# Optimization experiments

Measured on AMD Instinct MI355X. Metric: run time of the kernel, lower is better.

## Reference

```python
import jax, jax.numpy as jnp
import numpy as np

H = 6      # n_attention_heads
BLK = 64


def adder1x1(x2d, w):
    """AdderNet 1x1 'convolution': Y[co, n] = -sum_ci |x2d[ci, n] - w[co, ci]|.
    Processed in output-channel blocks to bound the abs-diff intermediate.
    x2d: [Ci, N], w: [Co, Ci] -> [Co, N]
    """
    co, ci = w.shape
    wb = w.reshape(co // BLK, BLK, ci)
    def f(wblk):  # wblk: [BLK, Ci] -> [BLK, N]
        return -jnp.sum(jnp.abs(x2d[None, :, :] - wblk[:, :, None]), axis=1)
    return jax.lax.map(f, wb).reshape(co, -1)


def layernorm_all(y, w, b, eps=1e-5):
    # nn.LayerNorm([E, B, S]) applied to [1, E, B, S]: normalize over ALL of E,B,S
    mu = jnp.mean(y)
    var = jnp.mean((y - mu) ** 2)
    return (y - mu) * jax.lax.rsqrt(var + eps) * w + b


def layernorm_last(y, w, b, eps=1e-5):
    mu = jnp.mean(y, axis=-1, keepdims=True)
    var = jnp.mean((y - mu) ** 2, axis=-1, keepdims=True)
    return (y - mu) * jax.lax.rsqrt(var + eps) * w + b


def setup_inputs() -> dict:
    key = jax.random.key(0)
    ks = jax.random.split(key, 14)
    B, S, E = 8, 197, 384
    inp = {
        "x": jax.random.normal(ks[0], (B, S, E), jnp.float32),
        "wq": jax.random.normal(ks[1], (E, E), jnp.float32) * 0.05,
        "wk": jax.random.normal(ks[2], (E, E), jnp.float32) * 0.05,
        "wv": jax.random.normal(ks[3], (E, E), jnp.float32) * 0.05,
        "qln_w": 1.0 + 0.02 * jax.random.normal(ks[4], (E, B, S), jnp.float32),
        "qln_b": 0.02 * jax.random.normal(ks[5], (E, B, S), jnp.float32),
        "kln_w": 1.0 + 0.02 * jax.random.normal(ks[6], (E, B, S), jnp.float32),
        "kln_b": 0.02 * jax.random.normal(ks[7], (E, B, S), jnp.float32),
        "vln_w": 1.0 + 0.02 * jax.random.normal(ks[8], (E, B, S), jnp.float32),
        "vln_b": 0.02 * jax.random.normal(ks[9], (E, B, S), jnp.float32),
        "oln_w": 1.0 + 0.02 * jax.random.normal(ks[10], (E,), jnp.float32),
        "oln_b": 0.02 * jax.random.normal(ks[11], (E,), jnp.float32),
        "fc_w": jax.random.normal(ks[12], (E, E), jnp.float32) * 0.05,
        "fc_b": 0.02 * jax.random.normal(ks[13], (E,), jnp.float32),
    }
    return inp


def reference(x, wq, wk, wv, qln_w, qln_b, kln_w, kln_b, vln_w, vln_b,
              oln_w, oln_b, fc_w, fc_b):
    B, S, E = x.shape
    D = E // H
    scale = (2.0 * D * (1.0 - 2.0 / np.pi)) ** (-0.5)

    # torch: x.reshape(1, E, B, S) on contiguous [B,S,E] is a flat-buffer reshape
    x2d = x.reshape(E, B * S)  # [Ci, N]

    def proj(w, lw, lb):
        y = adder1x1(x2d, w).reshape(E, B, S)          # adder2d 1x1, bias=False
        y = layernorm_all(y, lw, lb)                    # LN over [E,B,S]
        y = y.reshape(B, S, H, D)                       # flat reshape (as torch)
        y = jnp.swapaxes(y, 1, 2)                       # [B,H,S,D]
        return y.reshape(B * H, S, D)

    q = proj(wq, qln_w, qln_b)
    k = proj(wk, kln_w, kln_b)
    v = proj(wv, vln_w, vln_b)

    att = jnp.einsum('bsd,btd->bst', q, k) * scale      # [B*H, S, S]
    att = jax.nn.softmax(att, axis=-1) + jnp.eye(S, dtype=x.dtype)
    o = jnp.einsum('bst,btd->bsd', att, v)              # [B*H, S, D]

    o = jnp.swapaxes(o.reshape(B, H, S, D), 1, 2).reshape(B, S, E)
    o = layernorm_last(o, oln_w, oln_b)
    return o @ fc_w.T + fc_b
```

## Files before the change

### kernel.cpp

```cpp
#include <hip/hip_runtime.h>
#include <math.h>

#ifndef M_PI
#define M_PI 3.14159265358979323846
#endif

#define B_ 8
#define S_ 197
#define E_ 384
#define H_ 6
#define D_ 64
#define N_ (B_*S_)
#define EN ((size_t)E_*N_)
#define NBLK_RED 591

__global__ __launch_bounds__(256) void k_adder(
    const float* __restrict__ x,
    const float* __restrict__ wq, const float* __restrict__ wk,
    const float* __restrict__ wv,
    float* __restrict__ P)
{
  const int z = blockIdx.z;
  const int p = z >> 2, c = z & 3;
  const float* __restrict__ w = (p == 0) ? wq : (p == 1) ? wk : wv;
  const int co0 = blockIdx.x * 64;
  const int n0  = blockIdx.y * 64;
  const int cib = c * 96;

  __shared__ float Xs[2][16][68];
  __shared__ float Ws[2][16][68];

  const int tid = threadIdx.x;
  const int tx = tid & 15;
  const int ty = tid >> 4;

  const int xr = tid >> 4, xc = (tid & 15) * 4;
  const int wr = tid >> 2, wc = (tid & 3) * 4;

  const bool xok = (n0 + xc + 3) < N_;
  const float* xg = x + (size_t)(cib + xr) * N_ + n0 + xc;
  const float* wg = w + (size_t)(co0 + wr) * E_ + cib + wc;

  float4 xv = xok ? *(const float4*)xg : make_float4(0.f, 0.f, 0.f, 0.f);
  float4 wv4 = *(const float4*)wg;

  float acc[4][4];
  #pragma unroll
  for (int i = 0; i < 4; ++i)
    #pragma unroll
    for (int j = 0; j < 4; ++j) acc[i][j] = 0.f;

  #pragma unroll 1
  for (int t = 0; t < 6; ++t) {
    const int buf = t & 1;
    *(float4*)(&Xs[buf][xr][xc]) = xv;
    Ws[buf][wc + 0][wr] = wv4.x; Ws[buf][wc + 1][wr] = wv4.y;
    Ws[buf][wc + 2][wr] = wv4.z; Ws[buf][wc + 3][wr] = wv4.w;
    __syncthreads();
    if (t < 5) {
      xg += (size_t)16 * N_;
      wg += 16;
      xv = xok ? *(const float4*)xg : make_float4(0.f, 0.f, 0.f, 0.f);
      wv4 = *(const float4*)wg;
    }
    #pragma unroll
    for (int cc = 0; cc < 16; ++cc) {
      float4 a = *(const float4*)(&Xs[buf][cc][tx * 4]);
      float4 b = *(const float4*)(&Ws[buf][cc][ty * 4]);
      float xa[4] = {a.x, a.y, a.z, a.w};
      float wa[4] = {b.x, b.y, b.z, b.w};
      #pragma unroll
      for (int i = 0; i < 4; ++i)
        #pragma unroll
        for (int j = 0; j < 4; ++j)
          acc[i][j] += fabsf(xa[j] - wa[i]);
    }
  }

  if ((n0 + tx * 4 + 3) < N_) {
    #pragma unroll
    for (int i = 0; i < 4; ++i) {
      int co = co0 + ty * 4 + i;
      float4 yv = make_float4(acc[i][0], acc[i][1], acc[i][2], acc[i][3]);
      *(float4*)(P + (size_t)z * EN + (size_t)co * N_ + n0 + tx * 4) = yv;
    }
  }
}

__global__ __launch_bounds__(256) void k_reduceY(
    float* __restrict__ wsbuf, float* __restrict__ partials)
{
  const int p = blockIdx.y;
  float* P0 = wsbuf + (size_t)(4 * p) * EN;
  const int tid = threadIdx.x;
  size_t i = ((size_t)blockIdx.x * 256 + tid) * 4;
  float4 a = *(const float4*)(P0 + i);
  float4 b = *(const float4*)(P0 + EN + i);
  float4 cc = *(const float4*)(P0 + 2 * EN + i);
  float4 d = *(const float4*)(P0 + 3 * EN + i);
  float4 y;
  y.x = -(a.x + b.x + cc.x + d.x);
  y.y = -(a.y + b.y + cc.y + d.y);
  y.z = -(a.z + b.z + cc.z + d.z);
  y.w = -(a.w + b.w + cc.w + d.w);
  *(float4*)(P0 + i) = y;
  float s1 = y.x + y.y + y.z + y.w;
  float s2 = y.x * y.x + y.y * y.y + y.z * y.z + y.w * y.w;
  #pragma unroll
  for (int off = 32; off > 0; off >>= 1) {
    s1 += __shfl_down(s1, off);
    s2 += __shfl_down(s2, off);
  }
  __shared__ float red[8];
  int wid = tid >> 6, lane = tid & 63;
  if (lane == 0) { red[wid * 2] = s1; red[wid * 2 + 1] = s2; }
  __syncthreads();
  if (tid == 0) {
    float t1 = red[0] + red[2] + red[4] + red[6];
    float t2 = red[1] + red[3] + red[5] + red[7];
    partials[((size_t)p * NBLK_RED + blockIdx.x) * 2 + 0] = t1;
    partials[((size_t)p * NBLK_RED + blockIdx.x) * 2 + 1] = t2;
  }
}

__global__ __launch_bounds__(256) void k_stats(
    const float* __restrict__ partials, float* __restrict__ stats)
{
  const int p = blockIdx.x;
  const int tid = threadIdx.x;
  float s1 = 0.f, s2 = 0.f;
  for (int i = tid; i < NBLK_RED; i += 256) {
    s1 += partials[((size_t)p * NBLK_RED + i) * 2 + 0];
    s2 += partials[((size_t)p * NBLK_RED + i) * 2 + 1];
  }
  #pragma unroll
  for (int off = 32; off > 0; off >>= 1) {
    s1 += __shfl_down(s1, off);
    s2 += __shfl_down(s2, off);
  }
  __shared__ float red[8];
  int wid = tid >> 6, lane = tid & 63;
  if (lane == 0) { red[wid * 2] = s1; red[wid * 2 + 1] = s2; }
  __syncthreads();
  if (tid == 0) {
    float S1 = red[0] + red[2] + red[4] + red[6];
    float S2 = red[1] + red[3] + red[5] + red[7];
    float mean = S1 / (float)EN;
    float var = S2 / (float)EN - mean * mean;
    stats[p * 2 + 0] = mean;
    stats[p * 2 + 1] = rsqrtf(var + 1e-5f);
  }
}

__global__ __launch_bounds__(256) void k_lnall(
    float* __restrict__ wsbuf, const float* __restrict__ stats,
    const float* __restrict__ w0, const float* __restrict__ b0,
    const float* __restrict__ w1, const float* __restrict__ b1,
    const float* __restrict__ w2, const float* __restrict__ b2)
{
  const int p = blockIdx.y;
  const float* __restrict__ w = (p == 0) ? w0 : (p == 1) ? w1 : w2;
  const float* __restrict__ b = (p == 0) ? b0 : (p == 1) ? b1 : b2;
  const float mean = stats[p * 2 + 0];
  const float rstd = stats[p * 2 + 1];
  size_t i = ((size_t)blockIdx.x * 256 + threadIdx.x) * 4;
  const float* Yp = wsbuf + (size_t)(4 * p) * EN;
  float* Zp = wsbuf + (size_t)(4 * p + 1) * EN;
  float4 y = *(const float4*)(Yp + i);
  float4 wv = *(const float4*)(w + i);
  float4 bv = *(const float4*)(b + i);
  float4 zv;
  zv.x = (y.x - mean) * rstd * wv.x + bv.x;
  zv.y = (y.y - mean) * rstd * wv.y + bv.y;
  zv.z = (y.z - mean) * rstd * wv.z + bv.z;
  zv.w = (y.w - mean) * rstd * wv.w + bv.w;
  *(float4*)(Zp + i) = zv;
}

__global__ __launch_bounds__(256) void k_attn(
    const float* __restrict__ zq, const float* __restrict__ zk,
    const float* __restrict__ zv, float* __restrict__ obuf, float scale)
{
  const int bh = blockIdx.x, b = bh / H_, h = bh % H_;
  const int s0 = blockIdx.y * 32;

  __shared__ float Qs[64][36];
  __shared__ float KVs[64][68];
  __shared__ float Ps[32][200];
  __shared__ float linv[32];

  const int tid = threadIdx.x;
  const int tx = tid & 15, ty = tid >> 4;

  #pragma unroll
  for (int it = 0; it < 2; ++it) {
    int idx = tid + it * 256;
    int sl = idx >> 4, c4 = (idx & 15) * 4;
    int s = s0 + sl;
    float4 v = make_float4(0.f, 0.f, 0.f, 0.f);
    if (s < S_) v = *(const float4*)(zq + (size_t)(b * S_ + s) * E_ + h * D_ + c4);
    Qs[c4 + 0][sl] = v.x; Qs[c4 + 1][sl] = v.y;
    Qs[c4 + 2][sl] = v.z; Qs[c4 + 3][sl] = v.w;
  }

  float accS[4][2][4];
  #pragma unroll
  for (int tt = 0; tt < 4; ++tt)
    #pragma unroll
    for (int r = 0; r < 2; ++r)
      #pragma unroll
      for (int j = 0; j < 4; ++j) accS[tt][r][j] = 0.f;

  #pragma unroll
  for (int tt = 0; tt < 4; ++tt) {
    __syncthreads();
    #pragma unroll
    for (int it = 0; it < 4; ++it) {
      int idx = tid + it * 256;
      int tl = idx >> 4, c4 = (idx & 15) * 4;
      int t = tt * 64 + tl;
      float4 u = make_float4(0.f, 0.f, 0.f, 0.f);
      if (t < S_) u = *(const float4*)(zk + (size_t)(b * S_ + t) * E_ + h * D_ + c4);
      KVs[c4 + 0][tl] = u.x; KVs[c4 + 1][tl] = u.y;
      KVs[c4 + 2][tl] = u.z; KVs[c4 + 3][tl] = u.w;
    }
    __syncthreads();
    #pragma unroll 8
    for (int d = 0; d < 64; ++d) {
      float2 q2 = *(const float2*)(&Qs[d][2 * ty]);
      float4 k4 = *(const float4*)(&KVs[d][tx * 4]);
      float ka[4] = {k4.x, k4.y, k4.z, k4.w};
      #pragma unroll
      for (int j = 0; j < 4; ++j) {
        accS[tt][0][j] += q2.x * ka[j];
        accS[tt][1][j] += q2.y * ka[j];
      }
    }
  }

  float mr0 = -1e30f, mr1 = -1e30f;
  #pragma unroll
  for (int tt = 0; tt < 4; ++tt)
    #pragma unroll
    for (int j = 0; j < 4; ++j) {
      int t = tt * 64 + tx * 4 + j;
      float v0 = (t < S_) ? accS[tt][0][j] * scale : -1e30f;
      float v1 = (t < S_) ? accS[tt][1][j] * scale : -1e30f;
      accS[tt][0][j] = v0; accS[tt][1][j] = v1;
      mr0 = fmaxf(mr0, v0); mr1 = fmaxf(mr1, v1);
    }
  #pragma unroll
  for (int off = 1; off < 16; off <<= 1) {
    mr0 = fmaxf(mr0, __shfl_xor(mr0, off));
    mr1 = fmaxf(mr1, __shfl_xor(mr1, off));
  }
  float sr0 = 0.f, sr1 = 0.f;
  #pragma unroll
  for (int tt = 0; tt < 4; ++tt)
    #pragma unroll
    for (int j = 0; j < 4; ++j) {
      float p0 = __expf(accS[tt][0][j] - mr0);
      float p1 = __expf(accS[tt][1][j] - mr1);
      accS[tt][0][j] = p0; accS[tt][1][j] = p1;
      sr0 += p0; sr1 += p1;
    }
  #pragma unroll
  for (int off = 1; off < 16; off <<= 1) {
    sr0 += __shfl_xor(sr0, off);
    sr1 += __shfl_xor(sr1, off);
  }
  if (tx == 0) { linv[2 * ty] = 1.f / sr0; linv[2 * ty + 1] = 1.f / sr1; }
  #pragma unroll
  for (int tt = 0; tt < 4; ++tt) {
    int t4 = tt * 64 + tx * 4;
    if (t4 < 200) {
      *(float4*)(&Ps[2 * ty][t4]) =
          make_float4(accS[tt][0][0], accS[tt][0][1], accS[tt][0][2], accS[tt][0][3]);
      *(float4*)(&Ps[2 * ty + 1][t4]) =
          make_float4(accS[tt][1][0], accS[tt][1][1], accS[tt][1][2], accS[tt][1][3]);
    }
  }

  float accO[2][4];
  #pragma unroll
  for (int r = 0; r < 2; ++r)
    #pragma unroll
    for (int j = 0; j < 4; ++j) accO[r][j] = 0.f;

  #pragma unroll
  for (int tt = 0; tt < 4; ++tt) {
    __syncthreads();
    #pragma unroll
    for (int it = 0; it < 4; ++it) {
      int idx = tid + it * 256;
      int tl = idx >> 4, c4 = (idx & 15) * 4;
      int t = tt * 64 + tl;
      float4 u = make_float4(0.f, 0.f, 0.f, 0.f);
      if (t < S_) u = *(const float4*)(zv + (size_t)(b * S_ + t) * E_ + h * D_ + c4);
      *(float4*)(&KVs[tl][c4]) = u;
    }
    __syncthreads();
    const int tmax = (tt < 3) ? 64 : 8;
    #pragma unroll 8
    for (int tl = 0; tl < tmax; ++tl) {
      float p0 = Ps[2 * ty][tt * 64 + tl];
      float p1 = Ps[2 * ty + 1][tt * 64 + tl];
      float4 v4 = *(const float4*)(&KVs[tl][tx * 4]);
      float va[4] = {v4.x, v4.y, v4.z, v4.w};
      #pragma unroll
      for (int j = 0; j < 4; ++j) {
        accO[0][j] += p0 * va[j];
        accO[1][j] += p1 * va[j];
      }
    }
  }

  #pragma unroll
  for (int r = 0; r < 2; ++r) {
    int s = s0 + 2 * ty + r;
    if (s < S_) {
      float inv = linv[2 * ty + r];
      float4 vs = *(const float4*)(zv + (size_t)(b * S_ + s) * E_ + h * D_ + tx * 4);
      float4 o;
      o.x = accO[r][0] * inv + vs.x;
      o.y = accO[r][1] * inv + vs.y;
      o.z = accO[r][2] * inv + vs.z;
      o.w = accO[r][3] * inv + vs.w;
      *(float4*)(obuf + (size_t)(b * S_ + s) * E_ + h * D_ + tx * 4) = o;
    }
  }
}

__global__ __launch_bounds__(256) void k_lnlast(
    const float* __restrict__ obuf,
    const float* __restrict__ lw, const float* __restrict__ lb,
    float* __restrict__ oln)
{
  const int row = blockIdx.x * 4 + (threadIdx.x >> 6);
  const int lane = threadIdx.x & 63;
  const float* base = obuf + (size_t)row * E_;
  float v[6];
  float s1 = 0.f;
  #pragma unroll
  for (int j = 0; j < 6; ++j) { v[j] = base[lane + 64 * j]; s1 += v[j]; }
  #pragma unroll
  for (int off = 32; off > 0; off >>= 1) s1 += __shfl_xor(s1, off);
  float mean = s1 * (1.f / E_);
  float s2 = 0.f;
  #pragma unroll
  for (int j = 0; j < 6; ++j) { float d = v[j] - mean; s2 += d * d; }
  #pragma unroll
  for (int off = 32; off > 0; off >>= 1) s2 += __shfl_xor(s2, off);
  float rstd = rsqrtf(s2 * (1.f / E_) + 1e-5f);
  float* ob = oln + (size_t)row * E_;
  #pragma unroll
  for (int j = 0; j < 6; ++j) {
    int e = lane + 64 * j;
    ob[e] = (v[j] - mean) * rstd * lw[e] + lb[e];
  }
}

__global__ __launch_bounds__(256) void k_fc(
    const float* __restrict__ oln, const float* __restrict__ fcw,
    const float* __restrict__ fcb, float* __restrict__ out)
{
  const int j0 = blockIdx.x * 64, n0 = blockIdx.y * 32;
  __shared__ float Xs[16][36];
  __shared__ float Ws[16][68];
  const int tid = threadIdx.x;
  const int tx = tid & 15, ty = tid >> 4;
  float acc[4][2];
  #pragma unroll
  for (int i = 0; i < 4; ++i) { acc[i][0] = 0.f; acc[i][1] = 0.f; }

  for (int e0 = 0; e0 < E_; e0 += 16) {
    {
      int nl = tid >> 3, e2 = (tid & 7) * 2;
      int n = n0 + nl;
      float2 v = make_float2(0.f, 0.f);
      if (n < N_) v = *(const float2*)(oln + (size_t)n * E_ + e0 + e2);
      Xs[e2 + 0][nl] = v.x; Xs[e2 + 1][nl] = v.y;
      int jl = tid >> 2, c4 = (tid & 3) * 4;
      float4 u = *(const float4*)(fcw + (size_t)(j0 + jl) * E_ + e0 + c4);
      Ws[c4 + 0][jl] = u.x; Ws[c4 + 1][jl] = u.y;
      Ws[c4 + 2][jl] = u.z; Ws[c4 + 3][jl] = u.w;
    }
    __syncthreads();
    #pragma unroll
    for (int cc = 0; cc < 16; ++cc) {
      float2 x2 = *(const float2*)(&Xs[cc][tx * 2]);
      float4 w4 = *(const float4*)(&Ws[cc][ty * 4]);
      float xa[2] = {x2.x, x2.y};
      float wa[4] = {w4.x, w4.y, w4.z, w4.w};
      #pragma unroll
      for (int i = 0; i < 4; ++i) {
        acc[i][0] += wa[i] * xa[0];
        acc[i][1] += wa[i] * xa[1];
      }
    }
    __syncthreads();
  }
  const int jc = j0 + ty * 4;
  float4 bv = *(const float4*)(fcb + jc);
  #pragma unroll
  for (int jn = 0; jn < 2; ++jn) {
    int n = n0 + tx * 2 + jn;
    if (n < N_) {
      float4 o;
      o.x = acc[0][jn] + bv.x;
      o.y = acc[1][jn] + bv.y;
      o.z = acc[2][jn] + bv.z;
      o.w = acc[3][jn] + bv.w;
      *(float4*)(out + (size_t)n * E_ + jc) = o;
    }
  }
}

extern "C" void kernel_launch(void* const* d_in, const int* in_sizes, int n_in,
                              void* d_out, int out_size, void* d_ws, size_t ws_size,
                              hipStream_t stream)
{
  const float* x   = (const float*)d_in[0];
  const float* wq  = (const float*)d_in[1];
  const float* wk  = (const float*)d_in[2];
  const float* wv  = (const float*)d_in[3];
  const float* qw  = (const float*)d_in[4];
  const float* qb  = (const float*)d_in[5];
  const float* kw  = (const float*)d_in[6];
  const float* kb  = (const float*)d_in[7];
  const float* vw  = (const float*)d_in[8];
  const float* vb  = (const float*)d_in[9];
  const float* ow  = (const float*)d_in[10];
  const float* obp = (const float*)d_in[11];
  const float* fcw = (const float*)d_in[12];
  const float* fcb = (const float*)d_in[13];
  float* out = (float*)d_out;
  float* ws  = (float*)d_ws;

  float* obuf  = ws + 0 * EN;
  float* oln   = ws + 2 * EN;
  float* part  = ws + 12 * EN;
  float* stats = part + 3 * NBLK_RED * 2;

  const float scale = (float)pow(2.0 * D_ * (1.0 - 2.0 / M_PI), -0.5);

  k_adder<<<dim3(6, 25, 12), 256, 0, stream>>>(x, wq, wk, wv, ws);
  k_reduceY<<<dim3(NBLK_RED, 3), 256, 0, stream>>>(ws, part);
  k_stats<<<dim3(3), 256, 0, stream>>>(part, stats);
  k_lnall<<<dim3(NBLK_RED, 3), 256, 0, stream>>>(ws, stats, qw, qb, kw, kb, vw, vb);
  const float* zq = ws + 1 * EN;
  const float* zk = ws + 5 * EN;
  const float* zv = ws + 9 * EN;
  k_attn<<<dim3(48, 7), 256, 0, stream>>>(zq, zk, zv, obuf, scale);
  k_lnlast<<<dim3(394), 256, 0, stream>>>(obuf, ow, obp, oln);
  k_fc<<<dim3(6, 50), 256, 0, stream>>>(oln, fcw, fcb, out);
}
```

Before: 113.7 us.

## Enlarge adder tile to 128 output channels and add 8-way split-K

New measurement: 146.5 us. 1.29x slower.

```diff
diff --git a/kernel.cpp b/kernel.cpp
--- a/kernel.cpp
+++ b/kernel.cpp
@@ -14,95 +14,116 @@
 #define EN ((size_t)E_*N_)
 #define NBLK_RED 591
 
+template<int NS>
 __global__ __launch_bounds__(256) void k_adder(
     const float* __restrict__ x,
     const float* __restrict__ wq, const float* __restrict__ wk,
     const float* __restrict__ wv,
     float* __restrict__ P)
 {
+  constexpr int CHUNK = E_ / NS;
+  constexpr int STEPS = CHUNK / 16;
   const int z = blockIdx.z;
-  const int p = z >> 2, c = z & 3;
+  const int p = z / NS, c = z % NS;
   const float* __restrict__ w = (p == 0) ? wq : (p == 1) ? wk : wv;
-  const int co0 = blockIdx.x * 64;
+  const int co0 = blockIdx.x * 128;
   const int n0  = blockIdx.y * 64;
-  const int cib = c * 96;
+  const int cib = c * CHUNK;
 
   __shared__ float Xs[2][16][68];
-  __shared__ float Ws[2][16][68];
+  __shared__ float Ws[2][16][132];
 
   const int tid = threadIdx.x;
   const int tx = tid & 15;
   const int ty = tid >> 4;
 
   const int xr = tid >> 4, xc = (tid & 15) * 4;
-  const int wr = tid >> 2, wc = (tid & 3) * 4;
-
-  const bool xok = (n0 + xc + 3) < N_;
+  const int wco = tid >> 1, wci = (tid & 1) * 8;
+
+  const bool nok = (n0 + xc + 3) < N_;
   const float* xg = x + (size_t)(cib + xr) * N_ + n0 + xc;
-  const float* wg = w + (size_t)(co0 + wr) * E_ + cib + wc;
-
-  float4 xv = xok ? *(const float4*)xg : make_float4(0.f, 0.f, 0.f, 0.f);
-  float4 wv4 = *(const float4*)wg;
-
-  float acc[4][4];
-  #pragma unroll
-  for (int i = 0; i < 4; ++i)
+  const float* wg = w + (size_t)(co0 + wco) * E_ + cib + wci;
+
+  const float4 zero4 = make_float4(0.f, 0.f, 0.f, 0.f);
+  float4 xv  = nok ? *(const float4*)xg : zero4;
+  float4 wv0 = *(const float4*)wg;
+  float4 wv1 = *(const float4*)(wg + 4);
+
+  *(float4*)(&Xs[0][xr][xc]) = xv;
+  Ws[0][wci + 0][wco] = wv0.x; Ws[0][wci + 1][wco] = wv0.y;
+  Ws[0][wci + 2][wco] = wv0.z; Ws[0][wci + 3][wco] = wv0.w;
+  Ws[0][wci + 4][wco] = wv1.x; Ws[0][wci + 5][wco] = wv1.y;
+  Ws[0][wci + 6][wco] = wv1.z; Ws[0][wci + 7][wco] = wv1.w;
+
+  float acc[8][4];
+  #pragma unroll
+  for (int i = 0; i < 8; ++i)
     #pragma unroll
     for (int j = 0; j < 4; ++j) acc[i][j] = 0.f;
 
   #pragma unroll 1
-  for (int t = 0; t < 6; ++t) {
-    const int buf = t & 1;
-    *(float4*)(&Xs[buf][xr][xc]) = xv;
-    Ws[buf][wc + 0][wr] = wv4.x; Ws[buf][wc + 1][wr] = wv4.y;
-    Ws[buf][wc + 2][wr] = wv4.z; Ws[buf][wc + 3][wr] = wv4.w;
-    __syncthreads();
-    if (t < 5) {
+  for (int t = 0; t < STEPS; ++t) {
+    __syncthreads();
+    if (t + 1 < STEPS) {
       xg += (size_t)16 * N_;
       wg += 16;
-      xv = xok ? *(const float4*)xg : make_float4(0.f, 0.f, 0.f, 0.f);
-      wv4 = *(const float4*)wg;
-    }
+      xv  = nok ? *(const float4*)xg : zero4;
+      wv0 = *(const float4*)wg;
+      wv1 = *(const float4*)(wg + 4);
+    }
+    const int buf = t & 1;
     #pragma unroll
     for (int cc = 0; cc < 16; ++cc) {
-      float4 a = *(const float4*)(&Xs[buf][cc][tx * 4]);
-      float4 b = *(const float4*)(&Ws[buf][cc][ty * 4]);
+      float4 a  = *(const float4*)(&Xs[buf][cc][tx * 4]);
+      float4 wA = *(const float4*)(&Ws[buf][cc][ty * 4]);
+      float4 wB = *(const float4*)(&Ws[buf][cc][64 + ty * 4]);
       float xa[4] = {a.x, a.y, a.z, a.w};
-      float wa[4] = {b.x, b.y, b.z, b.w};
-      #pragma unroll
-      for (int i = 0; i < 4; ++i)
+      float wa[8] = {wA.x, wA.y, wA.z, wA.w, wB.x, wB.y, wB.z, wB.w};
+      #pragma unroll
+      for (int i = 0; i < 8; ++i)
         #pragma unroll
         for (int j = 0; j < 4; ++j)
           acc[i][j] += fabsf(xa[j] - wa[i]);
     }
-  }
-
-  if ((n0 + tx * 4 + 3) < N_) {
-    #pragma unroll
-    for (int i = 0; i < 4; ++i) {
-      int co = co0 + ty * 4 + i;
-      float4 yv = make_float4(acc[i][0], acc[i][1], acc[i][2], acc[i][3]);
-      *(float4*)(P + (size_t)z * EN + (size_t)co * N_ + n0 + tx * 4) = yv;
-    }
-  }
-}
-
+    if (t + 1 < STEPS) {
+      const int nb = (t + 1) & 1;
+      *(float4*)(&Xs[nb][xr][xc]) = xv;
+      Ws[nb][wci + 0][wco] = wv0.x; Ws[nb][wci + 1][wco] = wv0.y;
+      Ws[nb][wci + 2][wco] = wv0.z; Ws[nb][wci + 3][wco] = wv0.w;
+      Ws[nb][wci + 4][wco] = wv1.x; Ws[nb][wci + 5][wco] = wv1.y;
+      Ws[nb][wci + 6][wco] = wv1.z; Ws[nb][wci + 7][wco] = wv1.w;
+    }
+  }
+
+  if (nok) {
+    #pragma unroll
+    for (int ih = 0; ih < 2; ++ih) {
+      #pragma unroll
+      for (int r = 0; r < 4; ++r) {
+        const int co = co0 + ih * 64 + ty * 4 + r;
+        float4 yv = make_float4(acc[ih * 4 + r][0], acc[ih * 4 + r][1],
+                                acc[ih * 4 + r][2], acc[ih * 4 + r][3]);
+        *(float4*)(P + (size_t)z * EN + (size_t)co * N_ + n0 + tx * 4) = yv;
+      }
+    }
+  }
+}
+
+template<int NS>
 __global__ __launch_bounds__(256) void k_reduceY(
     float* __restrict__ wsbuf, float* __restrict__ partials)
 {
   const int p = blockIdx.y;
-  float* P0 = wsbuf + (size_t)(4 * p) * EN;
+  float* P0 = wsbuf + (size_t)(NS * p) * EN;
   const int tid = threadIdx.x;
   size_t i = ((size_t)blockIdx.x * 256 + tid) * 4;
-  float4 a = *(const float4*)(P0 + i);
-  float4 b = *(const float4*)(P0 + EN + i);
-  float4 cc = *(const float4*)(P0 + 2 * EN + i);
-  float4 d = *(const float4*)(P0 + 3 * EN + i);
-  float4 y;
-  y.x = -(a.x + b.x + cc.x + d.x);
-  y.y = -(a.y + b.y + cc.y + d.y);
-  y.z = -(a.z + b.z + cc.z + d.z);
-  y.w = -(a.w + b.w + cc.w + d.w);
+  float4 y = make_float4(0.f, 0.f, 0.f, 0.f);
+  #pragma unroll
+  for (int c = 0; c < NS; ++c) {
+    float4 a = *(const float4*)(P0 + (size_t)c * EN + i);
+    y.x += a.x; y.y += a.y; y.z += a.z; y.w += a.w;
+  }
+  y.x = -y.x; y.y = -y.y; y.z = -y.z; y.w = -y.w;
   *(float4*)(P0 + i) = y;
   float s1 = y.x + y.y + y.z + y.w;
   float s2 = y.x * y.x + y.y * y.y + y.z * y.z + y.w * y.w;
@@ -156,7 +177,7 @@
     float* __restrict__ wsbuf, const float* __restrict__ stats,
     const float* __restrict__ w0, const float* __restrict__ b0,
     const float* __restrict__ w1, const float* __restrict__ b1,
-    const float* __restrict__ w2, const float* __restrict__ b2)
+    const float* __restrict__ w2, const float* __restrict__ b2, int nslot)
 {
   const int p = blockIdx.y;
   const float* __restrict__ w = (p == 0) ? w0 : (p == 1) ? w1 : w2;
@@ -164,8 +185,8 @@
   const float mean = stats[p * 2 + 0];
   const float rstd = stats[p * 2 + 1];
   size_t i = ((size_t)blockIdx.x * 256 + threadIdx.x) * 4;
-  const float* Yp = wsbuf + (size_t)(4 * p) * EN;
-  float* Zp = wsbuf + (size_t)(4 * p + 1) * EN;
+  const float* Yp = wsbuf + (size_t)(nslot * p) * EN;
+  float* Zp = wsbuf + (size_t)(nslot * p + 1) * EN;
   float4 y = *(const float4*)(Yp + i);
   float4 wv = *(const float4*)(w + i);
   float4 bv = *(const float4*)(b + i);
@@ -437,20 +458,28 @@
   float* out = (float*)d_out;
   float* ws  = (float*)d_ws;
 
+  const size_t need8 = (24 * EN + 3 * NBLK_RED * 2 + 64) * sizeof(float);
+  const int NS = (ws_size >= need8) ? 8 : 4;
+
   float* obuf  = ws + 0 * EN;
   float* oln   = ws + 2 * EN;
-  float* part  = ws + 12 * EN;
+  float* part  = ws + (size_t)(3 * NS) * EN;
   float* stats = part + 3 * NBLK_RED * 2;
 
   const float scale = (float)pow(2.0 * D_ * (1.0 - 2.0 / M_PI), -0.5);
 
-  k_adder<<<dim3(6, 25, 12), 256, 0, stream>>>(x, wq, wk, wv, ws);
-  k_reduceY<<<dim3(NBLK_RED, 3), 256, 0, stream>>>(ws, part);
+  if (NS == 8) {
+    k_adder<8><<<dim3(3, 25, 24), 256, 0, stream>>>(x, wq, wk, wv, ws);
+    k_reduceY<8><<<dim3(NBLK_RED, 3), 256, 0, stream>>>(ws, part);
+  } else {
+    k_adder<4><<<dim3(3, 25, 12), 256, 0, stream>>>(x, wq, wk, wv, ws);
+    k_reduceY<4><<<dim3(NBLK_RED, 3), 256, 0, stream>>>(ws, part);
+  }
   k_stats<<<dim3(3), 256, 0, stream>>>(part, stats);
-  k_lnall<<<dim3(NBLK_RED, 3), 256, 0, stream>>>(ws, stats, qw, qb, kw, kb, vw, vb);
-  const float* zq = ws + 1 * EN;
-  const float* zk = ws + 5 * EN;
-  const float* zv = ws + 9 * EN;
+  k_lnall<<<dim3(NBLK_RED, 3), 256, 0, stream>>>(ws, stats, qw, qb, kw, kb, vw, vb, NS);
+  const float* zq = ws + (size_t)(0 * NS + 1) * EN;
+  const float* zk = ws + (size_t)(1 * NS + 1) * EN;
+  const float* zv = ws + (size_t)(2 * NS + 1) * EN;
   k_attn<<<dim3(48, 7), 256, 0, stream>>>(zq, zk, zv, obuf, scale);
   k_lnlast<<<dim3(394), 256, 0, stream>>>(obuf, ow, obp, oln);
   k_fc<<<dim3(6, 50), 256, 0, stream>>>(oln, fcw, fcb, out);
```
